# Kernel tuning notes

Hardware: AMD Instinct MI355X
Metric: run time of the kernel (lower is better)

Reference implementation:

```python
import jax, jax.numpy as jnp
import numpy as np

N = 16_777_216  # total nodes
B = 16_384      # graphs per batch


def setup_inputs() -> dict:
    key = jax.random.key(0)
    ks = jax.random.split(key, 9)
    x = jax.random.normal(ks[0], (N, 1), dtype=jnp.float32)
    batch = jnp.sort(jax.random.randint(ks[1], (N,), 0, B)).astype(jnp.int64)
    node_type = jax.random.randint(ks[2], (N,), 0, 3).astype(jnp.int64)
    # MLP params (torch Linear default-ish init scale)
    W1 = jax.random.normal(ks[3], (4, 32), dtype=jnp.float32) * 0.5
    b1 = jax.random.normal(ks[4], (32,), dtype=jnp.float32) * 0.1
    W2 = jax.random.normal(ks[5], (32, 16), dtype=jnp.float32) * 0.18
    b2 = jax.random.normal(ks[6], (16,), dtype=jnp.float32) * 0.1
    W3 = jax.random.normal(ks[7], (16, 1), dtype=jnp.float32) * 0.25
    b3 = jax.random.normal(ks[8], (1,), dtype=jnp.float32) * 0.1
    return {"x": x, "batch": batch, "node_type": node_type, "num_graphs": B,
            "W1": W1, "b1": b1, "W2": W2, "b2": b2, "W3": W3, "b3": b3}


def reference(x, batch, node_type, num_graphs, W1, b1, W2, b2, W3, b3):
    # Per-graph node-type histogram: one fused segment pass over (N, 4)
    # columns = [count(nt==0), count(nt==1), count(nt==2), total_nodes]
    onehot = jax.nn.one_hot(node_type, 3, dtype=jnp.float32)           # (N, 3)
    per_node = jnp.concatenate([onehot, jnp.ones((onehot.shape[0], 1), jnp.float32)], axis=1)  # (N, 4)
    feats = jax.ops.segment_sum(per_node, batch, num_segments=num_graphs)  # (B, 4)
    feats = feats - jnp.array([54.5, 0.0, 0.0, 56.5], dtype=jnp.float32)
    h = jax.nn.relu(feats @ W1 + b1)
    h = jax.nn.relu(h @ W2 + b2)
    return h @ W3 + b3  # (B, 1)
```

## Files before the change

### kernel.cpp

```cpp
#include <hip/hip_runtime.h>


constexpr int GPW = 4;

__global__ __launch_bounds__(256) void fused_kernel(
    const int* __restrict__ batch, const int* __restrict__ ntype,
    const float* __restrict__ W1, const float* __restrict__ b1,
    const float* __restrict__ W2, const float* __restrict__ b2,
    const float* __restrict__ W3, const float* __restrict__ b3,
    float* __restrict__ out, int n, int B)
{
    __shared__ float sW1[128], sW2[512], sb1[32], sb2[16], sW3[16], sb3v[1];
    const int tid = threadIdx.x;
    if (tid < 128) sW1[tid] = W1[tid];
    sW2[tid] = W2[tid];
    sW2[tid + 256] = W2[tid + 256];
    if      (tid < 32)  sb1[tid]      = b1[tid];
    else if (tid < 48)  sb2[tid - 32] = b2[tid - 32];
    else if (tid < 64)  sW3[tid - 48] = W3[tid - 48];
    else if (tid == 64) sb3v[0]       = b3[0];
    __syncthreads();

    const int wid  = (blockIdx.x * 256 + tid) >> 6;
    const int lane = tid & 63;
    const int g0   = wid * GPW;
    if (g0 >= B) return;

    int ans = 0;
    if (lane <= GPW) {
        const int g = min(g0 + lane, B);
        const long long c = (long long)g * (long long)(n / B);
        long long Wn = 8192;
        int lo, hi;
        for (;;) {
            long long l = c - Wn; if (l < 0) l = 0;
            long long h = c + Wn + 3; if (h > n) h = n;
            lo = (int)l & ~3;
            hi = (int)h & ~3;
            const bool okL = (lo == 0) || (batch[lo - 1] < g);
            const bool okR = (hi == n) || (batch[hi] >= g);
            if (okL && okR) break;
            Wn <<= 2;
        }
        while (hi - lo > 4) {
            const int mid = ((lo + hi) >> 1) & ~3;
            const int4 q = *(const int4*)(batch + mid);
            if (q.w < g)       lo = mid + 4;
            else if (q.x >= g) hi = mid;
            else { lo = mid; hi = mid + 4; }
        }
        ans = lo;
        if (lo < hi) {
            const int4 q = *(const int4*)(batch + lo);
            ans = lo + (q.x < g) + (q.y < g) + (q.z < g) + (q.w < g);
        }
    }

    for (int i = 0; i < GPW; ++i) {
        const int g = g0 + i;
        if (g >= B) break;
        const int s   = __shfl(ans, i);
        const int e   = __shfl(ans, i + 1);
        const int len = e - s;

        int c0 = 0, c1 = 0;
        int sa = (s + 3) & ~3; if (sa > e) sa = e;
        int ea = e & ~3;       if (ea < sa) ea = sa;

        {
            const int idx = s + lane;
            if (idx < sa) { const int v = ntype[idx]; c0 += (v == 0); c1 += (v == 1); }
        }
        {
            const int4* nt4 = (const int4*)ntype;
            for (int q = (sa >> 2) + lane; q < (ea >> 2); q += 64) {
                const int4 v = nt4[q];
                c0 += (v.x == 0) + (v.y == 0) + (v.z == 0) + (v.w == 0);
                c1 += (v.x == 1) + (v.y == 1) + (v.z == 1) + (v.w == 1);
            }
        }
        {
            const int idx = ea + lane;
            if (idx < e) { const int v = ntype[idx]; c0 += (v == 0); c1 += (v == 1); }
        }

        unsigned long long p = (unsigned)c0 | ((unsigned long long)(unsigned)c1 << 32);
        #pragma unroll
        for (int off = 32; off; off >>= 1) p += __shfl_xor(p, off);
        const int c0t = (int)(p & 0xFFFFFFFFull);
        const int c1t = (int)(p >> 32);

        const float f0 = (float)c0t - 54.5f;
        const float f1 = (float)c1t;
        const float f2 = (float)(len - c0t - c1t);
        const float f3 = (float)len - 56.5f;

        const int j = lane & 31;
        float h1 = sb1[j];
        h1 = fmaf(f0, sW1[      j], h1);
        h1 = fmaf(f1, sW1[ 32 + j], h1);
        h1 = fmaf(f2, sW1[ 64 + j], h1);
        h1 = fmaf(f3, sW1[ 96 + j], h1);
        h1 = fmaxf(0.0f, h1);

        const int m = lane & 15;
        float s2 = sb2[m];
        #pragma unroll
        for (int jj = 0; jj < 32; ++jj)
            s2 = fmaf(__shfl(h1, jj), sW2[jj * 16 + m], s2);
        const float h2 = fmaxf(0.0f, s2);

        float p3 = h2 * sW3[m];
        p3 += __shfl_xor(p3, 8);
        p3 += __shfl_xor(p3, 4);
        p3 += __shfl_xor(p3, 2);
        p3 += __shfl_xor(p3, 1);

        if (lane == 0) out[g] = p3 + sb3v[0];
    }
}

extern "C" void kernel_launch(void* const* d_in, const int* in_sizes, int n_in,
                              void* d_out, int out_size, void* d_ws, size_t ws_size,
                              hipStream_t stream) {
    const int*   batch = (const int*)d_in[1];
    const int*   ntype = (const int*)d_in[2];
    const float* W1    = (const float*)d_in[4];
    const float* b1    = (const float*)d_in[5];
    const float* W2    = (const float*)d_in[6];
    const float* b2    = (const float*)d_in[7];
    const float* W3    = (const float*)d_in[8];
    const float* b3    = (const float*)d_in[9];
    float*       out   = (float*)d_out;

    const int n = in_sizes[1];
    const int B = out_size;

    const int waves  = (B + GPW - 1) / GPW;
    const int blocks = (waves * 64 + 255) / 256;
    fused_kernel<<<blocks, 256, 0, stream>>>(
        batch, ntype, W1, b1, W2, b2, W3, b3, out, n, B);
}
```

Baseline: 29.40 us.

## Split segment-bound search into separate kernel and use half-wave per graph

Moves the per-graph binary search for segment boundaries into its own kernel that writes the offsets to workspace. The main kernel then reads those offsets and gives each graph to half a wavefront (32 lanes), so a wave handles two graphs at once instead of looping over four. The node-type counting loop is unrolled ten times with clamped loads so more memory requests are in flight together. This costs an extra kernel launch and a workspace round trip in exchange for more parallelism and more memory-level parallelism.

```diff
diff --git a/kernel.cpp b/kernel.cpp
--- a/kernel.cpp
+++ b/kernel.cpp
@@ -1,10 +1,43 @@
 #include <hip/hip_runtime.h>
 
 
-constexpr int GPW = 4;
+__global__ __launch_bounds__(64) void bounds_kernel(
+    const int* __restrict__ batch, int* __restrict__ S, int n, int B)
+{
+    const int g = blockIdx.x * 64 + threadIdx.x;
+    if (g > B) return;
+    const long long c = (long long)g * (long long)(n / B);
+    long long Wn = 6144;
+    int lo, hi;
+    for (;;) {
+        long long l = c - Wn; if (l < 0) l = 0;
+        long long h = c + Wn + 3; if (h > n) h = n;
+        lo = (int)l & ~3;
+        hi = (int)h & ~3;
+        const bool okL = (lo == 0) || (batch[lo - 1] < g);
+        const bool okR = (hi == n) || (batch[hi] >= g);
+        if (okL && okR) break;
+        Wn <<= 2;
+    }
+    while (hi - lo > 4) {
+        const int mid = ((lo + hi) >> 1) & ~3;
+        const int4 q = *(const int4*)(batch + mid);
+        if (q.w < g)       lo = mid + 4;
+        else if (q.x >= g) hi = mid;
+        else { lo = mid; hi = mid + 4; }
+    }
+    int ans = lo;
+    if (lo < hi) {
+        const int4 q = *(const int4*)(batch + lo);
+        ans = lo + (q.x < g) + (q.y < g) + (q.z < g) + (q.w < g);
+    }
+    S[g] = ans;
+}
 
-__global__ __launch_bounds__(256) void fused_kernel(
-    const int* __restrict__ batch, const int* __restrict__ ntype,
+constexpr int UNR = 10;
+
+__global__ __launch_bounds__(256) void seg_mlp_kernel(
+    const int* __restrict__ ntype, const int* __restrict__ S,
     const float* __restrict__ W1, const float* __restrict__ b1,
     const float* __restrict__ W2, const float* __restrict__ b2,
     const float* __restrict__ W3, const float* __restrict__ b3,
@@ -13,7 +46,7 @@
     __shared__ float sW1[128], sW2[512], sb1[32], sb2[16], sW3[16], sb3v[1];
     const int tid = threadIdx.x;
     if (tid < 128) sW1[tid] = W1[tid];
-    sW2[tid] = W2[tid];
+    sW2[tid]       = W2[tid];
     sW2[tid + 256] = W2[tid + 256];
     if      (tid < 32)  sb1[tid]      = b1[tid];
     else if (tid < 48)  sb2[tid - 32] = b2[tid - 32];
@@ -21,103 +54,85 @@
     else if (tid == 64) sb3v[0]       = b3[0];
     __syncthreads();
 
+    const int lane = tid & 63;
+    const int half = lane >> 5;
+    const int l32  = lane & 31;
     const int wid  = (blockIdx.x * 256 + tid) >> 6;
-    const int lane = tid & 63;
-    const int g0   = wid * GPW;
-    if (g0 >= B) return;
+    const int g    = wid * 2 + half;
+    const bool valid = (g < B);
+    const int gg   = valid ? g : (B - 1);
 
-    int ans = 0;
-    if (lane <= GPW) {
-        const int g = min(g0 + lane, B);
-        const long long c = (long long)g * (long long)(n / B);
-        long long Wn = 8192;
-        int lo, hi;
-        for (;;) {
-            long long l = c - Wn; if (l < 0) l = 0;
-            long long h = c + Wn + 3; if (h > n) h = n;
-            lo = (int)l & ~3;
-            hi = (int)h & ~3;
-            const bool okL = (lo == 0) || (batch[lo - 1] < g);
-            const bool okR = (hi == n) || (batch[hi] >= g);
-            if (okL && okR) break;
-            Wn <<= 2;
-        }
-        while (hi - lo > 4) {
-            const int mid = ((lo + hi) >> 1) & ~3;
-            const int4 q = *(const int4*)(batch + mid);
-            if (q.w < g)       lo = mid + 4;
-            else if (q.x >= g) hi = mid;
-            else { lo = mid; hi = mid + 4; }
-        }
-        ans = lo;
-        if (lo < hi) {
-            const int4 q = *(const int4*)(batch + lo);
-            ans = lo + (q.x < g) + (q.y < g) + (q.z < g) + (q.w < g);
-        }
+    const int s   = S[gg];
+    const int e   = S[gg + 1];
+    const int len = e - s;
+
+    int c0 = 0, c1 = 0;
+    int sa = (s + 3) & ~3; if (sa > e) sa = e;
+    int ea = e & ~3;       if (ea < sa) ea = sa;
+
+    {
+        const int i = s + l32;
+        if (i < sa) { const int v = ntype[i]; c0 += (v == 0); c1 += (v == 1); }
     }
-
-    for (int i = 0; i < GPW; ++i) {
-        const int g = g0 + i;
-        if (g >= B) break;
-        const int s   = __shfl(ans, i);
-        const int e   = __shfl(ans, i + 1);
-        const int len = e - s;
-
-        int c0 = 0, c1 = 0;
-        int sa = (s + 3) & ~3; if (sa > e) sa = e;
-        int ea = e & ~3;       if (ea < sa) ea = sa;
-
-        {
-            const int idx = s + lane;
-            if (idx < sa) { const int v = ntype[idx]; c0 += (v == 0); c1 += (v == 1); }
-        }
-        {
-            const int4* nt4 = (const int4*)ntype;
-            for (int q = (sa >> 2) + lane; q < (ea >> 2); q += 64) {
-                const int4 v = nt4[q];
+    {
+        const int4* nt4 = (const int4*)ntype;
+        const int nqm1 = (n >> 2) - 1;
+        const int q0 = (sa >> 2) + l32;
+        const int qe = (ea >> 2);
+        #pragma unroll
+        for (int u = 0; u < UNR; ++u) {
+            const int qi = q0 + u * 32;
+            const int4 v = nt4[min(qi, nqm1)];
+            if (qi < qe) {
                 c0 += (v.x == 0) + (v.y == 0) + (v.z == 0) + (v.w == 0);
                 c1 += (v.x == 1) + (v.y == 1) + (v.z == 1) + (v.w == 1);
             }
         }
-        {
-            const int idx = ea + lane;
-            if (idx < e) { const int v = ntype[idx]; c0 += (v == 0); c1 += (v == 1); }
+        for (int qi = q0 + UNR * 32; qi < qe; qi += 32) {
+            const int4 v = nt4[qi];
+            c0 += (v.x == 0) + (v.y == 0) + (v.z == 0) + (v.w == 0);
+            c1 += (v.x == 1) + (v.y == 1) + (v.z == 1) + (v.w == 1);
         }
+    }
+    {
+        const int i = ea + l32;
+        if (i < e) { const int v = ntype[i]; c0 += (v == 0); c1 += (v == 1); }
+    }
 
-        unsigned long long p = (unsigned)c0 | ((unsigned long long)(unsigned)c1 << 32);
-        #pragma unroll
-        for (int off = 32; off; off >>= 1) p += __shfl_xor(p, off);
-        const int c0t = (int)(p & 0xFFFFFFFFull);
-        const int c1t = (int)(p >> 32);
+    unsigned long long p = (unsigned)c0 | ((unsigned long long)(unsigned)c1 << 32);
+    #pragma unroll
+    for (int off = 16; off; off >>= 1) p += __shfl_xor(p, off);
+    const int c0t = (int)(p & 0xFFFFFFFFull);
+    const int c1t = (int)(p >> 32);
 
-        const float f0 = (float)c0t - 54.5f;
-        const float f1 = (float)c1t;
-        const float f2 = (float)(len - c0t - c1t);
-        const float f3 = (float)len - 56.5f;
+    const float f0 = (float)c0t - 54.5f;
+    const float f1 = (float)c1t;
+    const float f2 = (float)(len - c0t - c1t);
+    const float f3 = (float)len - 56.5f;
 
-        const int j = lane & 31;
-        float h1 = sb1[j];
-        h1 = fmaf(f0, sW1[      j], h1);
-        h1 = fmaf(f1, sW1[ 32 + j], h1);
-        h1 = fmaf(f2, sW1[ 64 + j], h1);
-        h1 = fmaf(f3, sW1[ 96 + j], h1);
-        h1 = fmaxf(0.0f, h1);
+    const int j = l32;
+    float h1 = sb1[j];
+    h1 = fmaf(f0, sW1[      j], h1);
+    h1 = fmaf(f1, sW1[ 32 + j], h1);
+    h1 = fmaf(f2, sW1[ 64 + j], h1);
+    h1 = fmaf(f3, sW1[ 96 + j], h1);
+    h1 = fmaxf(0.0f, h1);
 
-        const int m = lane & 15;
-        float s2 = sb2[m];
-        #pragma unroll
-        for (int jj = 0; jj < 32; ++jj)
-            s2 = fmaf(__shfl(h1, jj), sW2[jj * 16 + m], s2);
-        const float h2 = fmaxf(0.0f, s2);
+    const int m = lane & 15;
+    const int hbase = lane & 32;
+    float s2 = sb2[m];
+    #pragma unroll
+    for (int jj = 0; jj < 32; ++jj)
+        s2 = fmaf(__shfl(h1, hbase + jj), sW2[jj * 16 + m], s2);
+    const float h2 = fmaxf(0.0f, s2);
 
-        float p3 = h2 * sW3[m];
-        p3 += __shfl_xor(p3, 8);
-        p3 += __shfl_xor(p3, 4);
-        p3 += __shfl_xor(p3, 2);
-        p3 += __shfl_xor(p3, 1);
+    float p3 = h2 * sW3[m];
+    p3 += __shfl_xor(p3, 8);
+    p3 += __shfl_xor(p3, 4);
+    p3 += __shfl_xor(p3, 2);
+    p3 += __shfl_xor(p3, 1);
 
-        if (lane == 0) out[g] = p3 + sb3v[0];
-    }
+    if (valid && l32 == 0) out[g] = p3 + sb3v[0];
 }
 
 extern "C" void kernel_launch(void* const* d_in, const int* in_sizes, int n_in,
@@ -136,8 +151,12 @@
     const int n = in_sizes[1];
     const int B = out_size;
 
-    const int waves  = (B + GPW - 1) / GPW;
+    int* S = (int*)d_ws;
+
+    bounds_kernel<<<(B + 1 + 63) / 64, 64, 0, stream>>>(batch, S, n, B);
+
+    const int waves  = (B + 1) / 2;
     const int blocks = (waves * 64 + 255) / 256;
-    fused_kernel<<<blocks, 256, 0, stream>>>(
-        batch, ntype, W1, b1, W2, b2, W3, b3, out, n, B);
+    seg_mlp_kernel<<<blocks, 256, 0, stream>>>(
+        ntype, S, W1, b1, W2, b2, W3, b3, out, n, B);
 }
```

Measured after the change: 30.21 us. 1.03x slower.

## Split into streaming partial-count kernel plus bounds/MLP gather kernel

Applied to the files above, without the earlier changes.

Replaces the single fused kernel with two launches. The first computes segment boundaries in dedicated blocks while the other blocks stream node_type at full bandwidth, writing packed counts per 64-element chunk to workspace. The second kernel gives each graph one wave that sums the precomputed chunk partials, handles the ragged edges from raw node_type, and runs the MLP. The aim is to replace the per-graph irregular scans with one coalesced streaming pass, at the cost of an extra launch, a workspace round-trip and a hard-coded workspace layout that assumes n is a multiple of 4096.

```diff
diff --git a/kernel.cpp b/kernel.cpp
--- a/kernel.cpp
+++ b/kernel.cpp
@@ -1,36 +1,21 @@
 #include <hip/hip_runtime.h>
 
 
-constexpr int GPW = 4;
+constexpr int BB = 65;
 
-__global__ __launch_bounds__(256) void fused_kernel(
+__global__ __launch_bounds__(256) void k1_bounds_stream(
     const int* __restrict__ batch, const int* __restrict__ ntype,
-    const float* __restrict__ W1, const float* __restrict__ b1,
-    const float* __restrict__ W2, const float* __restrict__ b2,
-    const float* __restrict__ W3, const float* __restrict__ b3,
-    float* __restrict__ out, int n, int B)
+    int* __restrict__ S, unsigned long long* __restrict__ partial,
+    int n, int B)
 {
-    __shared__ float sW1[128], sW2[512], sb1[32], sb2[16], sW3[16], sb3v[1];
+    const int bid = blockIdx.x;
     const int tid = threadIdx.x;
-    if (tid < 128) sW1[tid] = W1[tid];
-    sW2[tid] = W2[tid];
-    sW2[tid + 256] = W2[tid + 256];
-    if      (tid < 32)  sb1[tid]      = b1[tid];
-    else if (tid < 48)  sb2[tid - 32] = b2[tid - 32];
-    else if (tid < 64)  sW3[tid - 48] = W3[tid - 48];
-    else if (tid == 64) sb3v[0]       = b3[0];
-    __syncthreads();
 
-    const int wid  = (blockIdx.x * 256 + tid) >> 6;
-    const int lane = tid & 63;
-    const int g0   = wid * GPW;
-    if (g0 >= B) return;
-
-    int ans = 0;
-    if (lane <= GPW) {
-        const int g = min(g0 + lane, B);
+    if (bid < BB) {
+        const int g = bid * 256 + tid;
+        if (g > B) return;
         const long long c = (long long)g * (long long)(n / B);
-        long long Wn = 8192;
+        long long Wn = 6144;
         int lo, hi;
         for (;;) {
             long long l = c - Wn; if (l < 0) l = 0;
@@ -49,75 +34,123 @@
             else if (q.x >= g) hi = mid;
             else { lo = mid; hi = mid + 4; }
         }
-        ans = lo;
+        int ans = lo;
         if (lo < hi) {
             const int4 q = *(const int4*)(batch + lo);
             ans = lo + (q.x < g) + (q.y < g) + (q.z < g) + (q.w < g);
         }
+        S[g] = ans;
+    } else {
+        const int w    = (bid - BB) * 4 + (tid >> 6);
+        const int lane = tid & 63;
+        const int ws   = w << 10;
+        if (ws >= n) return;
+
+        const int4* nt4 = (const int4*)ntype;
+        const int q0 = (ws >> 2) + lane;
+        #pragma unroll
+        for (int u = 0; u < 4; ++u) {
+            const int4 t = nt4[q0 + u * 64];
+            const unsigned c0 = (t.x == 0) + (t.y == 0) + (t.z == 0) + (t.w == 0);
+            const unsigned c1 = (t.x == 1) + (t.y == 1) + (t.z == 1) + (t.w == 1);
+            unsigned long long p = (unsigned long long)c0
+                                 | ((unsigned long long)c1 << 32);
+            p += __shfl_xor(p, 1);
+            p += __shfl_xor(p, 2);
+            p += __shfl_xor(p, 4);
+            p += __shfl_xor(p, 8);
+            if ((lane & 15) == 0)
+                partial[w * 16 + u * 4 + (lane >> 4)] = p;
+        }
+    }
+}
+
+__global__ __launch_bounds__(256) void k2_gather_mlp(
+    const int* __restrict__ ntype, const int* __restrict__ S,
+    const unsigned long long* __restrict__ partial,
+    const float* __restrict__ W1, const float* __restrict__ b1,
+    const float* __restrict__ W2, const float* __restrict__ b2,
+    const float* __restrict__ W3, const float* __restrict__ b3,
+    float* __restrict__ out, int B)
+{
+    __shared__ float sW1[128], sW2[512], sb1[32], sb2[16], sW3[16], sb3v[1];
+    const int tid = threadIdx.x;
+    if (tid < 128) sW1[tid] = W1[tid];
+    sW2[tid]       = W2[tid];
+    sW2[tid + 256] = W2[tid + 256];
+    if      (tid < 32)  sb1[tid]      = b1[tid];
+    else if (tid < 48)  sb2[tid - 32] = b2[tid - 32];
+    else if (tid < 64)  sW3[tid - 48] = W3[tid - 48];
+    else if (tid == 64) sb3v[0]       = b3[0];
+    __syncthreads();
+
+    const int lane = tid & 63;
+    const int g    = (blockIdx.x * 256 + tid) >> 6;
+    if (g >= B) return;
+
+    const int s   = S[g];
+    const int e   = S[g + 1];
+    const int len = e - s;
+
+    const int ca = (s + 63) & ~63;
+    const int fb = e & ~63;
+
+    unsigned long long acc = 0;
+
+    {
+        const int idx = (s & ~63) + lane;
+        const int lim = min(e, ca);
+        if (idx >= s && idx < lim) {
+            const int v = ntype[idx];
+            acc += (unsigned long long)(v == 0)
+                 | ((unsigned long long)(v == 1) << 32);
+        }
+    }
+    for (int i = (ca >> 6) + lane; i < (fb >> 6); i += 64)
+        acc += partial[i];
+    {
+        if (fb >= ca) {
+            const int idx = fb + lane;
+            if (idx < e) {
+                const int v = ntype[idx];
+                acc += (unsigned long long)(v == 0)
+                     | ((unsigned long long)(v == 1) << 32);
+            }
+        }
     }
 
-    for (int i = 0; i < GPW; ++i) {
-        const int g = g0 + i;
-        if (g >= B) break;
-        const int s   = __shfl(ans, i);
-        const int e   = __shfl(ans, i + 1);
-        const int len = e - s;
+    #pragma unroll
+    for (int off = 32; off; off >>= 1) acc += __shfl_xor(acc, off);
+    const int c0t = (int)(acc & 0xFFFFFFFFull);
+    const int c1t = (int)(acc >> 32);
 
-        int c0 = 0, c1 = 0;
-        int sa = (s + 3) & ~3; if (sa > e) sa = e;
-        int ea = e & ~3;       if (ea < sa) ea = sa;
+    const float f0 = (float)c0t - 54.5f;
+    const float f1 = (float)c1t;
+    const float f2 = (float)(len - c0t - c1t);
+    const float f3 = (float)len - 56.5f;
 
-        {
-            const int idx = s + lane;
-            if (idx < sa) { const int v = ntype[idx]; c0 += (v == 0); c1 += (v == 1); }
-        }
-        {
-            const int4* nt4 = (const int4*)ntype;
-            for (int q = (sa >> 2) + lane; q < (ea >> 2); q += 64) {
-                const int4 v = nt4[q];
-                c0 += (v.x == 0) + (v.y == 0) + (v.z == 0) + (v.w == 0);
-                c1 += (v.x == 1) + (v.y == 1) + (v.z == 1) + (v.w == 1);
-            }
-        }
-        {
-            const int idx = ea + lane;
-            if (idx < e) { const int v = ntype[idx]; c0 += (v == 0); c1 += (v == 1); }
-        }
+    const int j = lane & 31;
+    float h1 = sb1[j];
+    h1 = fmaf(f0, sW1[      j], h1);
+    h1 = fmaf(f1, sW1[ 32 + j], h1);
+    h1 = fmaf(f2, sW1[ 64 + j], h1);
+    h1 = fmaf(f3, sW1[ 96 + j], h1);
+    h1 = fmaxf(0.0f, h1);
 
-        unsigned long long p = (unsigned)c0 | ((unsigned long long)(unsigned)c1 << 32);
-        #pragma unroll
-        for (int off = 32; off; off >>= 1) p += __shfl_xor(p, off);
-        const int c0t = (int)(p & 0xFFFFFFFFull);
-        const int c1t = (int)(p >> 32);
+    const int m = lane & 15;
+    float s2 = sb2[m];
+    #pragma unroll
+    for (int jj = 0; jj < 32; ++jj)
+        s2 = fmaf(__shfl(h1, jj), sW2[jj * 16 + m], s2);
+    const float h2 = fmaxf(0.0f, s2);
 
-        const float f0 = (float)c0t - 54.5f;
-        const float f1 = (float)c1t;
-        const float f2 = (float)(len - c0t - c1t);
-        const float f3 = (float)len - 56.5f;
+    float p3 = h2 * sW3[m];
+    p3 += __shfl_xor(p3, 8);
+    p3 += __shfl_xor(p3, 4);
+    p3 += __shfl_xor(p3, 2);
+    p3 += __shfl_xor(p3, 1);
 
-        const int j = lane & 31;
-        float h1 = sb1[j];
-        h1 = fmaf(f0, sW1[      j], h1);
-        h1 = fmaf(f1, sW1[ 32 + j], h1);
-        h1 = fmaf(f2, sW1[ 64 + j], h1);
-        h1 = fmaf(f3, sW1[ 96 + j], h1);
-        h1 = fmaxf(0.0f, h1);
-
-        const int m = lane & 15;
-        float s2 = sb2[m];
-        #pragma unroll
-        for (int jj = 0; jj < 32; ++jj)
-            s2 = fmaf(__shfl(h1, jj), sW2[jj * 16 + m], s2);
-        const float h2 = fmaxf(0.0f, s2);
-
-        float p3 = h2 * sW3[m];
-        p3 += __shfl_xor(p3, 8);
-        p3 += __shfl_xor(p3, 4);
-        p3 += __shfl_xor(p3, 2);
-        p3 += __shfl_xor(p3, 1);
-
-        if (lane == 0) out[g] = p3 + sb3v[0];
-    }
+    if (lane == 0) out[g] = p3 + sb3v[0];
 }
 
 extern "C" void kernel_launch(void* const* d_in, const int* in_sizes, int n_in,
@@ -136,8 +169,13 @@
     const int n = in_sizes[1];
     const int B = out_size;
 
-    const int waves  = (B + GPW - 1) / GPW;
-    const int blocks = (waves * 64 + 255) / 256;
-    fused_kernel<<<blocks, 256, 0, stream>>>(
-        batch, ntype, W1, b1, W2, b2, W3, b3, out, n, B);
+    int* S = (int*)d_ws;
+    unsigned long long* partial = (unsigned long long*)((char*)d_ws + 65664);
+
+    const int stream_blocks = (n >> 10) / 4;
+    k1_bounds_stream<<<BB + stream_blocks, 256, 0, stream>>>(
+        batch, ntype, S, partial, n, B);
+
+    k2_gather_mlp<<<(B * 64 + 255) / 256, 256, 0, stream>>>(
+        ntype, S, partial, W1, b1, W2, b2, W3, b3, out, B);
 }
```

After: 36.46 us. 1.24x slower.
